# Kernel optimization log

Measured on AMD Instinct MI355X. Metric: run time of the kernel, lower is better.

## Reference

```python
import jax, jax.numpy as jnp
import numpy as np

N = 50000      # nodes
E = 600000     # edges
G = 8          # graphs in the batch (for mean_nodes)
D = 128        # input_dim == hidden_dim
OUT = 10       # out_dim
NEG_SLOPE = 0.01  # nn.LeakyReLU default


def _lin(k, fi, fo):
    return jax.random.normal(k, (fi, fo), jnp.float32) / np.sqrt(fi).astype(np.float32)


def setup_inputs() -> dict:
    key = jax.random.key(0)
    ks = jax.random.split(key, 12)
    inputs = jax.random.normal(ks[0], (N, D), jnp.float32)
    src = jax.random.randint(ks[1], (E,), 0, N)
    dst = jax.random.randint(ks[2], (E,), 0, N)
    graph_id = jnp.sort(jax.random.randint(ks[3], (N,), 0, G))
    return {
        "inputs": inputs,
        "src": src,
        "dst": dst,
        "graph_id": graph_id,
        # GraphConv weights (DGL GraphConv: y = norm * A_norm x W + b)
        "W1": _lin(ks[4], D, D), "b1": jnp.zeros((D,), jnp.float32),
        "W2": _lin(ks[5], D, D), "b2": jnp.zeros((D,), jnp.float32),
        "W3": _lin(ks[6], D, D), "b3": jnp.zeros((D,), jnp.float32),
        # classifier head
        "Wc1": _lin(ks[7], D, 512),  "bc1": jnp.zeros((512,), jnp.float32),
        "Wc2": _lin(ks[8], 512, 256), "bc2": jnp.zeros((256,), jnp.float32),
        "Wc3": _lin(ks[9], 256, OUT), "bc3": jnp.zeros((OUT,), jnp.float32),
    }


def reference(inputs, src, dst, graph_id, W1, b1, W2, b2, W3, b3,
              Wc1, bc1, Wc2, bc2, Wc3, bc3):
    # DGL GraphConv with norm='both': h = D_in^{-1/2} A D_out^{-1/2} x W + b
    ones_e = jnp.ones((E,), jnp.float32)
    out_deg = jax.ops.segment_sum(ones_e, src, num_segments=N)
    in_deg = jax.ops.segment_sum(ones_e, dst, num_segments=N)
    src_norm = jnp.clip(out_deg, 1.0, None) ** -0.5   # [N]
    dst_norm = jnp.clip(in_deg, 1.0, None) ** -0.5    # [N]

    def gconv(x, W, b):
        x = x * src_norm[:, None]
        x = x @ W                                      # project first (in>=out)
        agg = jax.ops.segment_sum(x[src], dst, num_segments=N)  # SpMM
        return agg * dst_norm[:, None] + b

    h = gconv(inputs, W1, b1)
    h = gconv(h, W2, b2)
    h = gconv(h, W3, b3)

    # dgl.mean_nodes: per-graph mean over nodes
    sums = jax.ops.segment_sum(h, graph_id, num_segments=G)         # [G, D]
    cnts = jax.ops.segment_sum(jnp.ones((N,), jnp.float32), graph_id, num_segments=G)
    pooled = sums / jnp.clip(cnts, 1.0, None)[:, None]

    lrelu = lambda v: jax.nn.leaky_relu(v, NEG_SLOPE)
    x = lrelu(pooled @ Wc1 + bc1)
    x = lrelu(x @ Wc2 + bc2)
    x = lrelu(x @ Wc3 + bc3)
    return x
```

## Files before the change

### kernel.cpp

```cpp
#include <hip/hip_runtime.h>

#define Nn 50000
#define Ee 600000
#define Gg 8
#define Dd 128
#define NP 50048
#define NCHUNK 49

#define HWORDS 25024
#define HB 16
#define HIST_BLOCKS (2 * HB)
#define W12_BLOCKS 16
#define W123_BLOCKS 64
#define DTILE 64
#define DPBLK ((Nn + DTILE - 1) / DTILE)
#define RA_BLOCKS 128
#define RA_CHUNK ((DPBLK + RA_BLOCKS - 1) / RA_BLOCKS)

__global__ __launch_bounds__(1024) void hist_kernel(
    const int* __restrict__ src, const int* __restrict__ dst,
    unsigned int* __restrict__ phist,
    const float* __restrict__ W1, const float* __restrict__ W2,
    const float* __restrict__ W3, const float* __restrict__ b1,
    const float* __restrict__ b2,
    float* __restrict__ W12, float* __restrict__ e1, float* __restrict__ e2,
    int* __restrict__ accz)
{
    __shared__ unsigned int h[HWORDS];
    int t = threadIdx.x;
    int b = blockIdx.x;

    if (b < HIST_BLOCKS) {
        for (int i = t; i < HWORDS; i += 1024) h[i] = 0u;
        __syncthreads();
        int part = b >> 1;
        const int* arr = (b & 1) ? dst : src;
        int e0 = part * (Ee / HB);
        int eN = e0 + (Ee / HB);
        for (int e = e0 + t; e < eN; e += 1024) {
            int n = arr[e];
            atomicAdd(&h[n >> 1], 1u << ((n & 1) << 4));
        }
        __syncthreads();
        unsigned int* out = phist + (size_t)b * HWORDS;
        for (int i = t; i < HWORDS; i += 1024) out[i] = h[i];
    } else if (b < HIST_BLOCKS + W12_BLOCKS) {
        int j = (b - HIST_BLOCKS) * 8 + (t & 7);
        int k = t >> 3;
        float a = 0.f;
#pragma unroll 8
        for (int m = 0; m < 128; ++m) a += W1[k * 128 + m] * W2[m * 128 + j];
        W12[k * 128 + j] = a;
    } else {
        if (t < 128) {
            float a = 0.f;
#pragma unroll 8
            for (int k = 0; k < 128; ++k) a += b1[k] * W2[k * 128 + t];
            e1[t] = a;
        } else if (t < 256) {
            int c = t - 128;
            float a = 0.f;
#pragma unroll 8
            for (int k = 0; k < 128; ++k) a += b2[k] * W3[k * 128 + c];
            e2[c] = a;
        } else if (t < 256 + 88) {
            accz[t - 256] = 0;
        }
    }
}

__global__ __launch_bounds__(256) void scan_fused(
    const unsigned int* __restrict__ phist, const int* __restrict__ gid,
    float* __restrict__ srcn, float* __restrict__ pq, float* __restrict__ z,
    int* __restrict__ cnt, int* __restrict__ row_ptr, int* __restrict__ cursor,
    int* __restrict__ fs,
    const float* __restrict__ W12, const float* __restrict__ W3,
    const float* __restrict__ e1,
    float* __restrict__ W123, float* __restrict__ e1b)
{
    int b = blockIdx.x, t = threadIdx.x;
    if (b < NCHUNK) {
        __shared__ int tsum[256];
        __shared__ int lc[Gg];
        __shared__ int sbase;
        if (t < Gg) lc[t] = 0;
        __syncthreads();

        int d4[4];
        int wbase = b * 512 + t * 2;
#pragma unroll
        for (int wi = 0; wi < 2; ++wi) {
            int w = wbase + wi;
            unsigned so0 = 0, so1 = 0, si0 = 0, si1 = 0;
            if (w < HWORDS) {
#pragma unroll
                for (int p = 0; p < HB; ++p) {
                    unsigned a  = phist[(size_t)(2 * p) * HWORDS + w];
                    unsigned bb = phist[(size_t)(2 * p + 1) * HWORDS + w];
                    so0 += a & 0xffffu; so1 += a >> 16;
                    si0 += bb & 0xffffu; si1 += bb >> 16;
                }
            }
#pragma unroll
            for (int hh = 0; hh < 2; ++hh) {
                int n = 2 * w + hh;
                unsigned so = hh ? so1 : so0, si = hh ? si1 : si0;
                int d = 0;
                if (n < Nn) {
                    d = (int)so;
                    float sn = 1.f / sqrtf(fmaxf((float)so, 1.f));
                    float dn = 1.f / sqrtf(fmaxf((float)si, 1.f));
                    srcn[n] = sn; pq[n] = sn * dn;
                    int g = gid[n];
                    atomicAdd(&lc[g], 1);
                    float zr[8];
#pragma unroll
                    for (int gg = 0; gg < 8; ++gg) zr[gg] = (gg == g) ? dn : 0.f;
                    *(float4*)(z + (size_t)n * 8)     = *(float4*)zr;
                    *(float4*)(z + (size_t)n * 8 + 4) = *(float4*)(zr + 4);
                }
                d4[wi * 2 + hh] = d;
            }
        }
        int s = (d4[0] + d4[1]) + (d4[2] + d4[3]);
        tsum[t] = s;
        __syncthreads();
        for (int off = 1; off < 256; off <<= 1) {
            int x = (t >= off) ? tsum[t - off] : 0;
            __syncthreads();
            tsum[t] += x;
            __syncthreads();
        }
        int run = tsum[t] - s;

        if (t == 0) {
            int total = tsum[255];
            atomicExch(&fs[b], (total << 1) | 1);
            int base = 0;
            for (int p = 0; p < b; ++p) {
                int r;
                do { r = atomicAdd(&fs[p], 0); } while (!(r & 1));
                base += (r >> 1);
            }
            sbase = base;
        }
        __syncthreads();

        int gpos = sbase + run;
#pragma unroll
        for (int i = 0; i < 4; ++i) {
            int n = b * 1024 + t * 4 + i;
            if (n < Nn) { row_ptr[n] = gpos; cursor[n] = gpos; }
            gpos += d4[i];
        }
        if (b == NCHUNK - 1 && t == 255) row_ptr[Nn] = Ee;
        __syncthreads();
        if (t < Gg && lc[t] > 0) atomicAdd(&cnt[t], lc[t]);
    } else if (b < NCHUNK + W123_BLOCKS) {
        int j = (b - NCHUNK) * 2 + (t & 1);
        int k = t >> 1;
        float a = 0.f;
#pragma unroll 8
        for (int m = 0; m < 128; ++m) a += W12[k * 128 + m] * W3[m * 128 + j];
        W123[k * 128 + j] = a;
    } else {
        if (t < 128) {
            float a = 0.f;
#pragma unroll 8
            for (int k = 0; k < 128; ++k) a += e1[k] * W3[k * 128 + t];
            e1b[t] = a;
        }
    }
}

__global__ __launch_bounds__(256) void fill_kernel(
    const int* __restrict__ src, const int* __restrict__ dst,
    int* __restrict__ cursor, int* __restrict__ csr_dst)
{
    int e = blockIdx.x * 256 + threadIdx.x;
    if (e >= Ee) return;
    int pos = atomicAdd(&cursor[src[e]], 1);
    csr_dst[pos] = dst[e];
}

__global__ __launch_bounds__(256) void bspmm_kernel(
    const float* __restrict__ uin, const int* __restrict__ row_ptr,
    const int* __restrict__ csr, const float* __restrict__ pqv,
    float* __restrict__ uout, const float* __restrict__ sn,
    float* __restrict__ pwout)
{
    int t = threadIdx.x;
    int g = t & 7;
    int m = blockIdx.x * 32 + (t >> 3);
    float acc = 0.f, snm = 0.f;
    if (m < Nn) {
        int beg = row_ptr[m], end = row_ptr[m + 1];
        int j = beg;
        float a0 = 0.f, a1 = 0.f, a2 = 0.f, a3 = 0.f;
        float a4 = 0.f, a5 = 0.f, a6 = 0.f, a7 = 0.f;
        for (; j + 7 < end; j += 8) {
            int i0 = csr[j],     i1 = csr[j + 1], i2 = csr[j + 2], i3 = csr[j + 3];
            int i4 = csr[j + 4], i5 = csr[j + 5], i6 = csr[j + 6], i7 = csr[j + 7];
            a0 += uin[(size_t)i0 * 8 + g]; a1 += uin[(size_t)i1 * 8 + g];
            a2 += uin[(size_t)i2 * 8 + g]; a3 += uin[(size_t)i3 * 8 + g];
            a4 += uin[(size_t)i4 * 8 + g]; a5 += uin[(size_t)i5 * 8 + g];
            a6 += uin[(size_t)i6 * 8 + g]; a7 += uin[(size_t)i7 * 8 + g];
        }
        for (; j + 3 < end; j += 4) {
            int i0 = csr[j], i1 = csr[j + 1], i2 = csr[j + 2], i3 = csr[j + 3];
            a0 += uin[(size_t)i0 * 8 + g]; a1 += uin[(size_t)i1 * 8 + g];
            a2 += uin[(size_t)i2 * 8 + g]; a3 += uin[(size_t)i3 * 8 + g];
        }
        for (; j < end; ++j) a0 += uin[(size_t)csr[j] * 8 + g];
        acc = ((a0 + a1) + (a2 + a3)) + ((a4 + a5) + (a6 + a7));
        uout[(size_t)m * 8 + g] = pqv[m] * acc;
        if (pwout) snm = sn[m];
    }
    if (pwout) {
        __shared__ float red[Gg];
        if (t < Gg) red[t] = 0.f;
        __syncthreads();
        float v = snm * acc;
        v += __shfl_xor(v, 8, 64);
        v += __shfl_xor(v, 16, 64);
        v += __shfl_xor(v, 32, 64);
        if ((t & 63) < 8) atomicAdd(&red[t & 7], v);
        __syncthreads();
        if (t < Gg) atomicAdd(&pwout[t], red[t]);
    }
}

__global__ __launch_bounds__(256) void dotpool_kernel(
    const float* __restrict__ x, const float* __restrict__ u2p,
    const float* __restrict__ sn,
    const int* __restrict__ row_ptr, const int* __restrict__ csr,
    float* __restrict__ partial)
{
    __shared__ float xs[DTILE][Dd];
    __shared__ float f[DTILE][Gg];
    int t = threadIdx.x;
    int n0 = blockIdx.x * DTILE;

    {
        const float4* x4 = (const float4*)x;
        float4* xs4 = (float4*)xs;
#pragma unroll
        for (int k = 0; k < 8; ++k) {
            int idx = t + 256 * k;
            int i = idx >> 5;
            int n = n0 + i;
            xs4[idx] = (n < Nn) ? x4[(size_t)n * 32 + (idx & 31)]
                                : make_float4(0.f, 0.f, 0.f, 0.f);
        }
    }

    {
        int i = t >> 2, sub = t & 3;
        int n = n0 + i;
        float ax = 0.f, ay = 0.f, s = 0.f;
        if (n < Nn) {
            s = sn[n];
            int beg = row_ptr[n], end = row_ptr[n + 1];
            int j = beg;
            float bx = 0.f, by = 0.f, cx = 0.f, cy = 0.f, dx = 0.f, dy = 0.f;
            for (; j + 3 < end; j += 4) {
                int i0 = csr[j], i1 = csr[j + 1], i2 = csr[j + 2], i3 = csr[j + 3];
                float2 u0 = *(const float2*)(u2p + (size_t)i0 * 8 + sub * 2);
                float2 u1 = *(const float2*)(u2p + (size_t)i1 * 8 + sub * 2);
                float2 u2 = *(const float2*)(u2p + (size_t)i2 * 8 + sub * 2);
                float2 u3 = *(const float2*)(u2p + (size_t)i3 * 8 + sub * 2);
                ax += u0.x; ay += u0.y; bx += u1.x; by += u1.y;
                cx += u2.x; cy += u2.y; dx += u3.x; dy += u3.y;
            }
            for (; j < end; ++j) {
                float2 u = *(const float2*)(u2p + (size_t)csr[j] * 8 + sub * 2);
                ax += u.x; ay += u.y;
            }
            ax += bx + cx + dx; ay += by + cy + dy;
        }
        f[i][sub * 2 + 0] = s * ax;
        f[i][sub * 2 + 1] = s * ay;
    }
    __syncthreads();

    {
        int g = t >> 5, c = t & 31;
        float4 acc = {0.f, 0.f, 0.f, 0.f};
#pragma unroll 8
        for (int i = 0; i < DTILE; ++i) {
            float fv = f[i][g];
            float4 xv = *(const float4*)&xs[i][c * 4];
            acc.x += fv * xv.x; acc.y += fv * xv.y;
            acc.z += fv * xv.z; acc.w += fv * xv.w;
        }
        *(float4*)(partial + (size_t)blockIdx.x * 1024 + g * 128 + c * 4) = acc;
    }
}

__global__ __launch_bounds__(256) void dotreduceA_kernel(
    const float* __restrict__ partial, float* __restrict__ partial2)
{
    int b = blockIdx.x, t = threadIdx.x;
    int p0 = b * RA_CHUNK;
    int p1 = p0 + RA_CHUNK; if (p1 > DPBLK) p1 = DPBLK;
    float a0 = 0.f, a1 = 0.f, a2 = 0.f, a3 = 0.f;
    for (int p = p0; p < p1; ++p) {
        const float* pp = partial + (size_t)p * 1024;
        a0 += pp[t];
        a1 += pp[t + 256];
        a2 += pp[t + 512];
        a3 += pp[t + 768];
    }
    float* o = partial2 + (size_t)b * 1024;
    o[t] = a0; o[t + 256] = a1; o[t + 512] = a2; o[t + 768] = a3;
}

__global__ __launch_bounds__(256) void redx0_kernel(
    const float* __restrict__ partial2, const float* __restrict__ pw1r,
    const float* __restrict__ pw2r, const int* __restrict__ cnt,
    const float* __restrict__ W123, const float* __restrict__ e1b,
    const float* __restrict__ e2, const float* __restrict__ b3,
    float* __restrict__ x0g)
{
    __shared__ float ps[256];
    int t = threadIdx.x;
    int o = blockIdx.x * 256 + t;
    float a0 = 0.f, a1 = 0.f, a2 = 0.f, a3 = 0.f;
#pragma unroll 4
    for (int b = 0; b < RA_BLOCKS; b += 4) {
        a0 += partial2[(size_t)(b + 0) * 1024 + o];
        a1 += partial2[(size_t)(b + 1) * 1024 + o];
        a2 += partial2[(size_t)(b + 2) * 1024 + o];
        a3 += partial2[(size_t)(b + 3) * 1024 + o];
    }
    ps[t] = (a0 + a1) + (a2 + a3);
    __syncthreads();

    int g = o >> 7, c = o & 127, gl = t >> 7;
    float a = 0.f;
#pragma unroll 8
    for (int k = 0; k < 128; ++k) a += ps[gl * 128 + k] * W123[k * 128 + c];
    float inv = 1.f / fmaxf((float)cnt[g], 1.f);
    x0g[o] = a * inv + (pw2r[g] * inv) * e1b[c] + (pw1r[g] * inv) * e2[c] + b3[c];
}

__global__ __launch_bounds__(256) void fc1_kernel(
    const float* __restrict__ x0g, const float* __restrict__ Wc1,
    const float* __restrict__ bc1, float* __restrict__ x1g)
{
    __shared__ float xs[Gg * 128];
    __shared__ float par[256];
    int t = threadIdx.x;
    for (int i = t; i < Gg * 128; i += 256) xs[i] = x0g[i];
    __syncthreads();
    int h = t >> 7, rem = t & 127;
    int g = rem >> 4, m = blockIdx.x * 16 + (rem & 15);
    int k0 = h * 64;
    float a = 0.f;
#pragma unroll 16
    for (int k = 0; k < 64; ++k) a += xs[g * 128 + k0 + k] * Wc1[(size_t)(k0 + k) * 512 + m];
    par[t] = a;
    __syncthreads();
    if (t < 128) {
        float v = par[t] + par[t + 128] + bc1[m];
        x1g[g * 512 + m] = v > 0.f ? v : 0.01f * v;
    }
}

__global__ __launch_bounds__(256) void fc2_kernel(
    const float* __restrict__ x1g, const float* __restrict__ Wc2,
    const float* __restrict__ bc2, float* __restrict__ x2g)
{
    __shared__ float xs[Gg * 512];
    __shared__ float par[256];
    int t = threadIdx.x;
    for (int i = t; i < Gg * 512; i += 256) xs[i] = x1g[i];
    __syncthreads();
    int q = t >> 6, rem = t & 63;
    int g = rem >> 3, m = blockIdx.x * 8 + (rem & 7);
    int k0 = q * 128;
    float a = 0.f;
#pragma unroll 16
    for (int k = 0; k < 128; ++k) a += xs[g * 512 + k0 + k] * Wc2[(size_t)(k0 + k) * 256 + m];
    par[t] = a;
    __syncthreads();
    if (t < 64) {
        float v = par[t] + par[t + 64] + par[t + 128] + par[t + 192] + bc2[m];
        x2g[g * 256 + m] = v > 0.f ? v : 0.01f * v;
    }
}

__global__ __launch_bounds__(640) void fc3_kernel(
    const float* __restrict__ x2g, const float* __restrict__ Wc3,
    const float* __restrict__ bc3, float* __restrict__ out)
{
    __shared__ float xs[Gg * 256];
    int t = threadIdx.x;
    for (int i = t; i < Gg * 256; i += 640) xs[i] = x2g[i];
    __syncthreads();
    int w = t >> 6, lane = t & 63;
    if (w < 10) {
        float acc[Gg];
#pragma unroll
        for (int g = 0; g < Gg; ++g) acc[g] = 0.f;
#pragma unroll
        for (int kk = 0; kk < 4; ++kk) {
            int k = lane + kk * 64;
            float wv = Wc3[(size_t)k * 10 + w];
#pragma unroll
            for (int g = 0; g < Gg; ++g) acc[g] += xs[g * 256 + k] * wv;
        }
#pragma unroll
        for (int g = 0; g < Gg; ++g) {
            float v = acc[g];
            for (int off = 32; off; off >>= 1) v += __shfl_down(v, off, 64);
            if (lane == 0) {
                v += bc3[w];
                out[g * 10 + w] = v > 0.f ? v : 0.01f * v;
            }
        }
    }
}

extern "C" void kernel_launch(void* const* d_in, const int* in_sizes, int n_in,
                              void* d_out, int out_size, void* d_ws, size_t ws_size,
                              hipStream_t stream)
{
    const float* inputs = (const float*)d_in[0];
    const int*   src    = (const int*)d_in[1];
    const int*   dst    = (const int*)d_in[2];
    const int*   gid    = (const int*)d_in[3];
    const float* W1  = (const float*)d_in[4];
    const float* b1  = (const float*)d_in[5];
    const float* W2  = (const float*)d_in[6];
    const float* b2  = (const float*)d_in[7];
    const float* W3  = (const float*)d_in[8];
    const float* b3  = (const float*)d_in[9];
    const float* Wc1 = (const float*)d_in[10];
    const float* bc1 = (const float*)d_in[11];
    const float* Wc2 = (const float*)d_in[12];
    const float* bc2 = (const float*)d_in[13];
    const float* Wc3 = (const float*)d_in[14];
    const float* bc3 = (const float*)d_in[15];

    int*   wi      = (int*)d_ws;
    int*   row_ptr = wi;
    int*   cursor  = row_ptr + NP;
    int*   csr_dst = cursor + NP;
    float* wf      = (float*)(csr_dst + Ee);
    float* srcn    = wf;
    float* pq      = srcn + NP;
    float* z       = pq + NP;
    float* u1      = z + (size_t)NP * 8;
    float* u2      = u1 + (size_t)NP * 8;
    float* partial = u2 + (size_t)NP * 8;
    float* partial2= partial + (size_t)DPBLK * 1024;
    float* pw1     = partial2 + (size_t)RA_BLOCKS * 1024;
    float* pw2     = pw1 + Gg;
    int*   cnt     = (int*)(pw2 + Gg);
    int*   fs      = cnt + Gg;
    float* W12v    = (float*)(fs + 64);
    float* W123v   = W12v + 128 * 128;
    float* e1v     = W123v + 128 * 128;
    float* e1bv    = e1v + 128;
    float* e2v     = e1bv + 128;
    float* x0g     = e2v + 128;
    float* x1g     = x0g + 1024;
    float* x2g     = x1g + 4096;
    unsigned int* phist = (unsigned int*)(x2g + 2048);

    hist_kernel<<<HIST_BLOCKS + W12_BLOCKS + 1, 1024, 0, stream>>>(
        src, dst, phist, W1, W2, W3, b1, b2, W12v, e1v, e2v, (int*)pw1);
    scan_fused<<<NCHUNK + W123_BLOCKS + 1, 256, 0, stream>>>(
        phist, gid, srcn, pq, z, cnt, row_ptr, cursor, fs,
        W12v, W3, e1v, W123v, e1bv);
    fill_kernel<<<(Ee + 255) / 256, 256, 0, stream>>>(src, dst, cursor, csr_dst);

    int bblocks = (Nn + 31) / 32;
    bspmm_kernel<<<bblocks, 256, 0, stream>>>(z, row_ptr, csr_dst, pq,
                                              u1, srcn, pw1);
    bspmm_kernel<<<bblocks, 256, 0, stream>>>(u1, row_ptr, csr_dst, pq,
                                              u2, srcn, pw2);

    dotpool_kernel<<<DPBLK, 256, 0, stream>>>(inputs, u2, srcn,
                                              row_ptr, csr_dst, partial);
    dotreduceA_kernel<<<RA_BLOCKS, 256, 0, stream>>>(partial, partial2);
    redx0_kernel<<<4, 256, 0, stream>>>(partial2, pw1, pw2, cnt,
                                        W123v, e1bv, e2v, b3, x0g);
    fc1_kernel<<<32, 256, 0, stream>>>(x0g, Wc1, bc1, x1g);
    fc2_kernel<<<32, 256, 0, stream>>>(x1g, Wc2, bc2, x2g);
    fc3_kernel<<<1, 640, 0, stream>>>(x2g, Wc3, bc3, (float*)d_out);
}
```

Baseline: 172.8 us.

## Parallelize scan prefix lookback, batch fill loads, fuse reduction with fc1

Three changes. In the decoupled-lookback scan, each predecessor's flag is now polled by its own thread instead of thread 0 walking them serially, and the totals are summed from shared memory. The CSR fill kernel now handles two edges per thread, loading both before issuing the atomics. The final partial reduction, W123 projection and first classifier layer are merged into one 32-block kernel, which drops one launch and the x0g round trip. In exchange, each block redundantly recomputes the reduction and projection for its graph row.

```diff
diff --git a/kernel.cpp b/kernel.cpp
--- a/kernel.cpp
+++ b/kernel.cpp
@@ -82,6 +82,7 @@
     if (b < NCHUNK) {
         __shared__ int tsum[256];
         __shared__ int lc[Gg];
+        __shared__ int pre[64];
         __shared__ int sbase;
         if (t < Gg) lc[t] = 0;
         __syncthreads();
@@ -133,15 +134,16 @@
         }
         int run = tsum[t] - s;
 
+        if (t == 0) atomicExch(&fs[b], (tsum[255] << 1) | 1);
+        if (t < b) {
+            int r;
+            do { r = atomicAdd(&fs[t], 0); } while (!(r & 1));
+            pre[t] = r >> 1;
+        }
+        __syncthreads();
         if (t == 0) {
-            int total = tsum[255];
-            atomicExch(&fs[b], (total << 1) | 1);
             int base = 0;
-            for (int p = 0; p < b; ++p) {
-                int r;
-                do { r = atomicAdd(&fs[p], 0); } while (!(r & 1));
-                base += (r >> 1);
-            }
+            for (int p = 0; p < b; ++p) base += pre[p];
             sbase = base;
         }
         __syncthreads();
@@ -177,10 +179,13 @@
     const int* __restrict__ src, const int* __restrict__ dst,
     int* __restrict__ cursor, int* __restrict__ csr_dst)
 {
-    int e = blockIdx.x * 256 + threadIdx.x;
-    if (e >= Ee) return;
-    int pos = atomicAdd(&cursor[src[e]], 1);
-    csr_dst[pos] = dst[e];
+    int e0 = blockIdx.x * 512 + threadIdx.x;
+    int e1 = e0 + 256;
+    int s0 = -1, d0 = 0, s1 = -1, d1 = 0;
+    if (e0 < Ee) { s0 = src[e0]; d0 = dst[e0]; }
+    if (e1 < Ee) { s1 = src[e1]; d1 = dst[e1]; }
+    if (s0 >= 0) { int p = atomicAdd(&cursor[s0], 1); csr_dst[p] = d0; }
+    if (s1 >= 0) { int p = atomicAdd(&cursor[s1], 1); csr_dst[p] = d1; }
 }
 
 __global__ __launch_bounds__(256) void bspmm_kernel(
@@ -315,55 +320,62 @@
     o[t] = a0; o[t + 256] = a1; o[t + 512] = a2; o[t + 768] = a3;
 }
 
-__global__ __launch_bounds__(256) void redx0_kernel(
+__global__ __launch_bounds__(256) void redfc1_kernel(
     const float* __restrict__ partial2, const float* __restrict__ pw1r,
     const float* __restrict__ pw2r, const int* __restrict__ cnt,
     const float* __restrict__ W123, const float* __restrict__ e1b,
     const float* __restrict__ e2, const float* __restrict__ b3,
-    float* __restrict__ x0g)
-{
-    __shared__ float ps[256];
-    int t = threadIdx.x;
-    int o = blockIdx.x * 256 + t;
-    float a0 = 0.f, a1 = 0.f, a2 = 0.f, a3 = 0.f;
-#pragma unroll 4
-    for (int b = 0; b < RA_BLOCKS; b += 4) {
-        a0 += partial2[(size_t)(b + 0) * 1024 + o];
-        a1 += partial2[(size_t)(b + 1) * 1024 + o];
-        a2 += partial2[(size_t)(b + 2) * 1024 + o];
-        a3 += partial2[(size_t)(b + 3) * 1024 + o];
-    }
-    ps[t] = (a0 + a1) + (a2 + a3);
-    __syncthreads();
-
-    int g = o >> 7, c = o & 127, gl = t >> 7;
-    float a = 0.f;
-#pragma unroll 8
-    for (int k = 0; k < 128; ++k) a += ps[gl * 128 + k] * W123[k * 128 + c];
-    float inv = 1.f / fmaxf((float)cnt[g], 1.f);
-    x0g[o] = a * inv + (pw2r[g] * inv) * e1b[c] + (pw1r[g] * inv) * e2[c] + b3[c];
-}
-
-__global__ __launch_bounds__(256) void fc1_kernel(
-    const float* __restrict__ x0g, const float* __restrict__ Wc1,
-    const float* __restrict__ bc1, float* __restrict__ x1g)
-{
-    __shared__ float xs[Gg * 128];
-    __shared__ float par[256];
-    int t = threadIdx.x;
-    for (int i = t; i < Gg * 128; i += 256) xs[i] = x0g[i];
-    __syncthreads();
-    int h = t >> 7, rem = t & 127;
-    int g = rem >> 4, m = blockIdx.x * 16 + (rem & 15);
-    int k0 = h * 64;
-    float a = 0.f;
-#pragma unroll 16
-    for (int k = 0; k < 64; ++k) a += xs[g * 128 + k0 + k] * Wc1[(size_t)(k0 + k) * 512 + m];
-    par[t] = a;
-    __syncthreads();
-    if (t < 128) {
-        float v = par[t] + par[t + 128] + bc1[m];
-        x1g[g * 512 + m] = v > 0.f ? v : 0.01f * v;
+    const float* __restrict__ Wc1, const float* __restrict__ bc1,
+    float* __restrict__ x1g)
+{
+    __shared__ float prow[128];
+    __shared__ float x0row[128];
+    __shared__ float psum[256];
+    int b = blockIdx.x, t = threadIdx.x;
+    int g = b >> 2, q = b & 3;
+
+    {
+        int k = t & 127, h = t >> 7;
+        float a0 = 0.f, a1 = 0.f;
+        int p0 = h * 64;
+        for (int p = p0; p < p0 + 64; p += 2) {
+            a0 += partial2[(size_t)p * 1024 + g * 128 + k];
+            a1 += partial2[(size_t)(p + 1) * 1024 + g * 128 + k];
+        }
+        psum[t] = a0 + a1;
+        __syncthreads();
+        if (t < 128) prow[t] = psum[t] + psum[t + 128];
+        __syncthreads();
+    }
+    {
+        int c = t & 127, h = t >> 7;
+        float a = 0.f;
+        int k0 = h * 64;
+#pragma unroll 8
+        for (int k = k0; k < k0 + 64; ++k) a += prow[k] * W123[k * 128 + c];
+        psum[t] = a;
+        __syncthreads();
+        if (t < 128) {
+            float inv = 1.f / fmaxf((float)cnt[g], 1.f);
+            x0row[t] = (psum[t] + psum[t + 128]) * inv
+                     + (pw2r[g] * inv) * e1b[t] + (pw1r[g] * inv) * e2[t] + b3[t];
+        }
+        __syncthreads();
+    }
+    {
+        int m = q * 128 + (t & 127), h = t >> 7;
+        float a = 0.f;
+        int k0 = h * 64;
+#pragma unroll 8
+        for (int k = k0; k < k0 + 64; ++k)
+            a += x0row[k] * Wc1[(size_t)k * 512 + m];
+        psum[t] = a;
+        __syncthreads();
+        if (t < 128) {
+            int m2 = q * 128 + t;
+            float v = psum[t] + psum[t + 128] + bc1[m2];
+            x1g[g * 512 + m2] = v > 0.f ? v : 0.01f * v;
+        }
     }
 }
 
@@ -464,8 +476,7 @@
     float* e1v     = W123v + 128 * 128;
     float* e1bv    = e1v + 128;
     float* e2v     = e1bv + 128;
-    float* x0g     = e2v + 128;
-    float* x1g     = x0g + 1024;
+    float* x1g     = e2v + 128;
     float* x2g     = x1g + 4096;
     unsigned int* phist = (unsigned int*)(x2g + 2048);
 
@@ -474,7 +485,7 @@
     scan_fused<<<NCHUNK + W123_BLOCKS + 1, 256, 0, stream>>>(
         phist, gid, srcn, pq, z, cnt, row_ptr, cursor, fs,
         W12v, W3, e1v, W123v, e1bv);
-    fill_kernel<<<(Ee + 255) / 256, 256, 0, stream>>>(src, dst, cursor, csr_dst);
+    fill_kernel<<<(Ee + 511) / 512, 256, 0, stream>>>(src, dst, cursor, csr_dst);
 
     int bblocks = (Nn + 31) / 32;
     bspmm_kernel<<<bblocks, 256, 0, stream>>>(z, row_ptr, csr_dst, pq,
@@ -485,9 +496,8 @@
     dotpool_kernel<<<DPBLK, 256, 0, stream>>>(inputs, u2, srcn,
                                               row_ptr, csr_dst, partial);
     dotreduceA_kernel<<<RA_BLOCKS, 256, 0, stream>>>(partial, partial2);
-    redx0_kernel<<<4, 256, 0, stream>>>(partial2, pw1, pw2, cnt,
-                                        W123v, e1bv, e2v, b3, x0g);
-    fc1_kernel<<<32, 256, 0, stream>>>(x0g, Wc1, bc1, x1g);
+    redfc1_kernel<<<32, 256, 0, stream>>>(partial2, pw1, pw2, cnt,
+                                          W123v, e1bv, e2v, b3, Wc1, bc1, x1g);
     fc2_kernel<<<32, 256, 0, stream>>>(x1g, Wc2, bc2, x2g);
     fc3_kernel<<<1, 640, 0, stream>>>(x2g, Wc3, bc3, (float*)d_out);
 }
```

New measurement: 171.3 us. About the same (-0.9%).
